# Optimization experiments

Hardware: AMD Instinct MI355X
Metric: run time of the kernel (lower is better)

Reference implementation:

```python
import jax, jax.numpy as jnp
import numpy as np

B, E, N, NREL, K, T, L = 8, 2000, 10000, 25, 16, 3, 32
TAU1 = 10.0

def _clip01(x):
    return jnp.clip(x, 0.0, 1.0)

def setup_inputs():
    key = jax.random.key(0)
    ks = jax.random.split(key, 10)
    ent = jax.random.randint(ks[0], (B,), 0, E)
    input_x = jnp.zeros((B, E), jnp.float32).at[jnp.arange(B), ent].set(1.0)
    tidx = jax.random.randint(ks[1], (E,), 0, K)
    type_mat = jnp.zeros((E, K), jnp.float32).at[jnp.arange(E), tidx].set(1.0)
    heads = jax.random.randint(ks[2], (N,), 0, E)
    tails = jax.random.randint(ks[3], (N,), 0, E)
    rels = jax.random.randint(ks[4], (N,), 0, NREL)
    e2triple = jnp.zeros((E, N), jnp.float32).at[heads, jnp.arange(N)].set(1.0)
    triple2e = jnp.zeros((N, E), jnp.float32).at[jnp.arange(N), tails].set(1.0)
    triple2r = jnp.zeros((N, NREL), jnp.float32).at[jnp.arange(N), rels].set(1.0)
    def ku(k, shape):
        fan_in = int(np.prod(shape[1:]))
        bnd = 1.0 / np.sqrt(fan_in)
        return jax.random.uniform(k, shape, jnp.float32, -bnd, bnd)
    w = ku(ks[5], (T, L, NREL))
    weight = ku(ks[6], (L, 1))
    h = jnp.ones((T, L, NREL - 1), jnp.float32)
    h_x = jnp.ones((L, NREL - 1), jnp.float32)
    h_type = ku(ks[7], (T, L, K))
    h_x_type = ku(ks[8], (L, K))
    alpha = jnp.ones((T, L), jnp.float32)
    beta = jnp.ones((T, L), jnp.float32)
    alpha_x = jnp.ones((L,), jnp.float32)
    beta_x = jnp.ones((L,), jnp.float32)
    return dict(input_x=input_x, type_mat=type_mat, e2triple=e2triple,
                triple2e=triple2e, triple2r=triple2r, w=w, weight=weight,
                h=h, h_x=h_x, h_type=h_type, h_x_type=h_x_type,
                alpha=alpha, beta=beta, alpha_x=alpha_x, beta_x=beta_x, flag=0)

def _forward(input_x, type_mat, e2triple, triple2e, triple2r, w, weight,
             h, h_x, h_type, h_x_type, alpha, beta, alpha_x, beta_x):
    # flag=False, is_training=False path of TCLMModel.forward
    Bb = input_x.shape[0]
    Nn, Ee = triple2e.shape
    Tt, Ll = alpha.shape
    nrel = w.shape[-1]
    half = (nrel - 1) // 2
    x_ori = input_x @ e2triple                      # [B,N]
    e2r = triple2e.T @ triple2r                     # [E,nrel]
    hidden_base = _clip01(e2r)[:, :-1]              # [E,nrel-1]
    hx_raw = _clip01(x_ori @ triple2r)              # [B,nrel]
    hidden_x_base = jnp.concatenate([hx_raw[:, half:-1], hx_raw[:, :half]], axis=-1)
    ax = _clip01(alpha_x / TAU1)
    bx = _clip01(beta_x / TAU1)
    gate_x = 1.0 - _clip01(ax + bx)                 # [L]
    hxp = _clip01(h_x / TAU1)                       # [L,nrel-1]
    hxtp = _clip01(h_x_type / TAU1)                 # [L,K]
    hidden_type_x = input_x @ (type_mat @ hxtp.T)   # [B,L]
    hx_lin = hidden_x_base @ hxp.T                  # [B,L]
    s = None
    for t in range(Tt):
        a = _clip01(alpha[t] / TAU1)                # [L]
        b = _clip01(beta[t] / TAU1)
        hp = _clip01(h[t] / TAU1)                   # [L,nrel-1]
        htp = _clip01(h_type[t] / TAU1)             # [L,K]
        hidden = _clip01(a[None] * (type_mat @ htp.T) + b[None] * (hidden_base @ hp.T))
        hidden = (hidden + (1.0 - _clip01(a + b))[None]).T        # [L,E]
        # note: original code uses alpha/beta (not alpha_x/beta_x) here; replicate
        hidden_x = _clip01(a[None] * hidden_type_x + b[None] * hx_lin) + gate_x[None]  # [B,L]
        w_probs = jax.nn.softmax(w[t], axis=-1)     # [L,nrel]
        srel = triple2r @ w_probs.T                 # [N,L]
        if t == 0:
            sc = x_ori[:, None, :] * srel.T[None]   # [B,L,N]
            s = (sc.reshape(-1, Nn) @ triple2e).reshape(Bb, Ll, Ee)
            s = s * hidden[None] * hidden_x[:, :, None]
        else:
            xprev = (s.reshape(-1, Ee) @ e2triple).reshape(Bb, Ll, Nn)
            sc = xprev * srel.T[None]               # [B,L,N]
            s = (sc.reshape(-1, Nn) @ triple2e).reshape(Bb, Ll, Ee)
            s = s * hidden[None]
    out = jnp.einsum('ble,lk->bek', s, jnp.tanh(weight))[..., 0]  # [B,E]
    return out

def reference(input_x, type_mat, e2triple, triple2e, triple2r, w, weight,
              h, h_x, h_type, h_x_type, alpha, beta, alpha_x, beta_x, flag):
    return _forward(input_x, type_mat, e2triple, triple2e, triple2r, w, weight,
                    h, h_x, h_type, h_x_type, alpha, beta, alpha_x, beta_x)
```

## Files before the change

### kernel.cpp

```cpp
#include <hip/hip_runtime.h>

#define B 8
#define E 2000
#define NTRI 10000
#define NRELS 25
#define KT 16
#define TT 3
#define LL 32
#define TAU1 10.0f

__device__ __forceinline__ float clip01(float x) { return fminf(fmaxf(x, 0.0f), 1.0f); }

__global__ void extract_all(const float4* __restrict__ e2t, const float4* __restrict__ t2e,
                            const float* __restrict__ t2r, const float4* __restrict__ ix,
                            const float4* __restrict__ tm,
                            unsigned int* __restrict__ packed, unsigned int* __restrict__ mask,
                            int* __restrict__ ent, int* __restrict__ tidx,
                            float4* __restrict__ out4) {
    const int gtid = blockIdx.x * blockDim.x + threadIdx.x;
    const int gs = gridDim.x * blockDim.x;

    for (int i = gtid; i < E * NTRI / 4; i += gs) {
        float4 v = e2t[i];
        if (v.x != 0.0f || v.y != 0.0f || v.z != 0.0f || v.w != 0.0f) {
            int f = i * 4;
#pragma unroll
            for (int k = 0; k < 4; k++) {
                float c = (k == 0) ? v.x : (k == 1) ? v.y : (k == 2) ? v.z : v.w;
                if (c != 0.0f) {
                    int a = f + k;
                    int head = a / NTRI;
                    int j = a - head * NTRI;
                    atomicOr(&packed[j], (unsigned int)head);
                }
            }
        }
    }

    for (int i = gtid; i < NTRI * E / 4; i += gs) {
        float4 v = t2e[i];
        if (v.x != 0.0f || v.y != 0.0f || v.z != 0.0f || v.w != 0.0f) {
            int f = i * 4;
#pragma unroll
            for (int k = 0; k < 4; k++) {
                float c = (k == 0) ? v.x : (k == 1) ? v.y : (k == 2) ? v.z : v.w;
                if (c != 0.0f) {
                    int a = f + k;
                    int j = a / E;
                    int tail = a - j * E;
                    int r = 0;
                    while (r < NRELS - 1 && t2r[j * NRELS + r] == 0.0f) r++;
                    atomicOr(&packed[j], ((unsigned int)tail << 11) | ((unsigned int)r << 22));
                    if (r < NRELS - 1) atomicOr(&mask[tail], 1u << r);
                }
            }
        }
    }

    for (int i = gtid; i < B * E / 4; i += gs) {
        float4 v = ix[i];
        if (v.x != 0.0f || v.y != 0.0f || v.z != 0.0f || v.w != 0.0f) {
            int f = i * 4;
#pragma unroll
            for (int k = 0; k < 4; k++) {
                float c = (k == 0) ? v.x : (k == 1) ? v.y : (k == 2) ? v.z : v.w;
                if (c != 0.0f) { int a = f + k; int b = a / E; ent[b] = a - b * E; }
            }
        }
    }

    for (int i = gtid; i < E * KT / 4; i += gs) {
        float4 v = tm[i];
        if (v.x != 0.0f || v.y != 0.0f || v.z != 0.0f || v.w != 0.0f) {
            int f = i * 4;
#pragma unroll
            for (int k = 0; k < 4; k++) {
                float c = (k == 0) ? v.x : (k == 1) ? v.y : (k == 2) ? v.z : v.w;
                if (c != 0.0f) { int a = f + k; int e = a / KT; tidx[e] = a - e * KT; }
            }
        }
    }

    float4 z = make_float4(0.f, 0.f, 0.f, 0.f);
    for (int i = gtid; i < B * E / 4; i += gs) out4[i] = z;
}

__global__ void __launch_bounds__(256) prop(
        const float* __restrict__ sprev, const unsigned int* __restrict__ packed,
        const int* __restrict__ ent, const int* __restrict__ tidx,
        const unsigned int* __restrict__ mask,
        const float* __restrict__ w, const float* __restrict__ h,
        const float* __restrict__ h_type, const float* __restrict__ alpha,
        const float* __restrict__ beta, const float* __restrict__ h_x,
        const float* __restrict__ h_x_type, const float* __restrict__ alpha_x,
        const float* __restrict__ beta_x, const float* __restrict__ weight,
        float* __restrict__ sout, float* __restrict__ out, int t) {
    __shared__ float prev[E];
    __shared__ float acc[E];
    __shared__ float wrow[NRELS];
    __shared__ float hp[NRELS - 1];
    __shared__ float htpL[KT];
    __shared__ unsigned int relflag;

    const int blk = blockIdx.x, b = blk >> 5, l = blk & 31, tid = threadIdx.x;
    const int ent_b = ent[b];
    const int tl = t * LL + l;

    if (t != 0) {
        const float* sp = sprev + (size_t)blk * E;
        for (int e = tid; e < E; e += 256) prev[e] = sp[e];
    }
    for (int e = tid; e < E; e += 256) acc[e] = 0.0f;
    if (tid == 0) {
        relflag = 0u;
        const float* wr = w + tl * NRELS;
        float mx = wr[0];
        for (int r = 1; r < NRELS; r++) mx = fmaxf(mx, wr[r]);
        float ex[NRELS], s = 0.0f;
        for (int r = 0; r < NRELS; r++) { ex[r] = expf(wr[r] - mx); s += ex[r]; }
        float inv = 1.0f / s;
        for (int r = 0; r < NRELS; r++) wrow[r] = ex[r] * inv;
    }
    if (tid < NRELS - 1) hp[tid] = clip01(h[tl * (NRELS - 1) + tid] / TAU1);
    if (tid < KT) htpL[tid] = clip01(h_type[tl * KT + tid] / TAU1);
    __syncthreads();

    const uint4* p4 = (const uint4*)packed;
    if (t == 0) {
        for (int i = tid; i < NTRI / 4; i += 256) {
            uint4 p = p4[i];
#pragma unroll
            for (int k = 0; k < 4; k++) {
                unsigned int pk = (k == 0) ? p.x : (k == 1) ? p.y : (k == 2) ? p.z : p.w;
                int head = pk & 2047;
                if (head == ent_b) {
                    unsigned int r = pk >> 22;
                    int tail = (pk >> 11) & 2047;
                    atomicAdd(&acc[tail], wrow[r]);
                    atomicOr(&relflag, 1u << r);
                }
            }
        }
    } else {
        for (int i = tid; i < NTRI / 4; i += 256) {
            uint4 p = p4[i];
#pragma unroll
            for (int k = 0; k < 4; k++) {
                unsigned int pk = (k == 0) ? p.x : (k == 1) ? p.y : (k == 2) ? p.z : p.w;
                float pv = prev[pk & 2047];
                if (pv != 0.0f) {
                    unsigned int r = pk >> 22;
                    int tail = (pk >> 11) & 2047;
                    atomicAdd(&acc[tail], pv * wrow[r]);
                }
            }
        }
    }
    __syncthreads();

    const float a = clip01(alpha[tl] / TAU1);
    const float bb = clip01(beta[tl] / TAU1);
    const float base = 1.0f - clip01(a + bb);

    float extra = 1.0f;
    if (t == 0) {
        unsigned int fl = relflag;
        float hxlin = 0.0f;
        for (int i = 0; i < NRELS - 1; i++) {
            int pi = (i < 12) ? (12 + i) : (i - 12);
            if ((fl >> pi) & 1u) hxlin += clip01(h_x[l * (NRELS - 1) + i] / TAU1);
        }
        float htx = clip01(h_x_type[l * KT + tidx[ent_b]] / TAU1);
        float ax = clip01(alpha_x[l] / TAU1), bx = clip01(beta_x[l] / TAU1);
        extra = clip01(a * htx + bb * hxlin) + (1.0f - clip01(ax + bx));
    }

    if (t == 2) {
        float tw = tanhf(weight[l]);
        for (int e = tid; e < E; e += 256) {
            unsigned int m = mask[e];
            float dot = 0.0f;
#pragma unroll
            for (int i = 0; i < NRELS - 1; i++) dot += ((m >> i) & 1u) ? hp[i] : 0.0f;
            float he = clip01(a * htpL[tidx[e]] + bb * dot) + base;
            atomicAdd(&out[b * E + e], acc[e] * he * tw);
        }
    } else {
        float* so = sout + (size_t)blk * E;
        for (int e = tid; e < E; e += 256) {
            unsigned int m = mask[e];
            float dot = 0.0f;
#pragma unroll
            for (int i = 0; i < NRELS - 1; i++) dot += ((m >> i) & 1u) ? hp[i] : 0.0f;
            float he = clip01(a * htpL[tidx[e]] + bb * dot) + base;
            so[e] = acc[e] * he * extra;
        }
    }
}

extern "C" void kernel_launch(void* const* d_in, const int* in_sizes, int n_in,
                              void* d_out, int out_size, void* d_ws, size_t ws_size,
                              hipStream_t stream) {
    const float* input_x  = (const float*)d_in[0];
    const float* type_mat = (const float*)d_in[1];
    const float* e2triple = (const float*)d_in[2];
    const float* triple2e = (const float*)d_in[3];
    const float* triple2r = (const float*)d_in[4];
    const float* w        = (const float*)d_in[5];
    const float* weight   = (const float*)d_in[6];
    const float* h        = (const float*)d_in[7];
    const float* h_x      = (const float*)d_in[8];
    const float* h_type   = (const float*)d_in[9];
    const float* h_x_type = (const float*)d_in[10];
    const float* alpha    = (const float*)d_in[11];
    const float* beta     = (const float*)d_in[12];
    const float* alpha_x  = (const float*)d_in[13];
    const float* beta_x   = (const float*)d_in[14];
    (void)in_sizes; (void)n_in; (void)out_size; (void)ws_size;

    char* ws = (char*)d_ws;
    size_t off = 0;
    auto alloc = [&](size_t bytes) -> void* {
        void* p = ws + off;
        off += (bytes + 255) & ~(size_t)255;
        return p;
    };
    unsigned int* packed = (unsigned int*)alloc(NTRI * sizeof(unsigned int));
    unsigned int* maskp  = (unsigned int*)alloc(E * sizeof(unsigned int));
    size_t zero_bytes = off;
    int*   ent  = (int*)alloc(B * sizeof(int));
    int*   tidx = (int*)alloc(E * sizeof(int));
    float* sA   = (float*)alloc((size_t)B * LL * E * sizeof(float));
    float* sB   = (float*)alloc((size_t)B * LL * E * sizeof(float));

    hipMemsetAsync(ws, 0, zero_bytes, stream);

    extract_all<<<8192, 256, 0, stream>>>((const float4*)e2triple, (const float4*)triple2e,
                                          triple2r, (const float4*)input_x, (const float4*)type_mat,
                                          packed, maskp, ent, tidx, (float4*)d_out);

    prop<<<B * LL, 256, 0, stream>>>(nullptr, packed, ent, tidx, maskp, w, h, h_type,
                                     alpha, beta, h_x, h_x_type, alpha_x, beta_x, weight,
                                     sA, (float*)d_out, 0);
    prop<<<B * LL, 256, 0, stream>>>(sA, packed, ent, tidx, maskp, w, h, h_type,
                                     alpha, beta, h_x, h_x_type, alpha_x, beta_x, weight,
                                     sB, (float*)d_out, 1);
    prop<<<B * LL, 256, 0, stream>>>(sB, packed, ent, tidx, maskp, w, h, h_type,
                                     alpha, beta, h_x, h_x_type, alpha_x, beta_x, weight,
                                     nullptr, (float*)d_out, 2);
}
```

Baseline: 250.1 us.

## Fuse three propagation hops into one kernel and batch extraction loads

Merges the three per-hop propagation launches into a single kernel in which each (batch, rule) block keeps its state vector in shared memory across hops. This removes the global round trips through the intermediate state buffers and two kernel launches. Entity masks and type indices are now cached in shared memory, and blocks grow to 512 threads. The extraction kernel now uses fewer blocks, with each thread issuing four independent float4 loads per iteration to raise memory-level parallelism over the large dense matrices. The extra shared memory per block may limit occupancy.

```diff
diff --git a/kernel.cpp b/kernel.cpp
--- a/kernel.cpp
+++ b/kernel.cpp
@@ -8,193 +8,227 @@
 #define TT 3
 #define LL 32
 #define TAU1 10.0f
+#define XBLK 2048
+#define XTHR 256
 
 __device__ __forceinline__ float clip01(float x) { return fminf(fmaxf(x, 0.0f), 1.0f); }
 
-__global__ void extract_all(const float4* __restrict__ e2t, const float4* __restrict__ t2e,
-                            const float* __restrict__ t2r, const float4* __restrict__ ix,
-                            const float4* __restrict__ tm,
-                            unsigned int* __restrict__ packed, unsigned int* __restrict__ mask,
-                            int* __restrict__ ent, int* __restrict__ tidx,
-                            float4* __restrict__ out4) {
-    const int gtid = blockIdx.x * blockDim.x + threadIdx.x;
-    const int gs = gridDim.x * blockDim.x;
-
-    for (int i = gtid; i < E * NTRI / 4; i += gs) {
-        float4 v = e2t[i];
-        if (v.x != 0.0f || v.y != 0.0f || v.z != 0.0f || v.w != 0.0f) {
-            int f = i * 4;
-#pragma unroll
-            for (int k = 0; k < 4; k++) {
-                float c = (k == 0) ? v.x : (k == 1) ? v.y : (k == 2) ? v.z : v.w;
-                if (c != 0.0f) {
-                    int a = f + k;
-                    int head = a / NTRI;
-                    int j = a - head * NTRI;
-                    atomicOr(&packed[j], (unsigned int)head);
-                }
-            }
-        }
-    }
-
-    for (int i = gtid; i < NTRI * E / 4; i += gs) {
-        float4 v = t2e[i];
-        if (v.x != 0.0f || v.y != 0.0f || v.z != 0.0f || v.w != 0.0f) {
-            int f = i * 4;
-#pragma unroll
-            for (int k = 0; k < 4; k++) {
-                float c = (k == 0) ? v.x : (k == 1) ? v.y : (k == 2) ? v.z : v.w;
-                if (c != 0.0f) {
-                    int a = f + k;
-                    int j = a / E;
-                    int tail = a - j * E;
-                    int r = 0;
-                    while (r < NRELS - 1 && t2r[j * NRELS + r] == 0.0f) r++;
-                    atomicOr(&packed[j], ((unsigned int)tail << 11) | ((unsigned int)r << 22));
-                    if (r < NRELS - 1) atomicOr(&mask[tail], 1u << r);
-                }
-            }
-        }
-    }
+__device__ __forceinline__ void proc_e2t(float4 v, int i, unsigned int* packed) {
+    if (v.x == 0.f && v.y == 0.f && v.z == 0.f && v.w == 0.f) return;
+    int f = i * 4;
+    float c[4] = {v.x, v.y, v.z, v.w};
+#pragma unroll
+    for (int k = 0; k < 4; k++)
+        if (c[k] != 0.f) {
+            int a = f + k;
+            int head = a / NTRI;
+            int j = a - head * NTRI;
+            atomicOr(&packed[j], (unsigned int)head);
+        }
+}
+
+__device__ __forceinline__ void proc_t2e(float4 v, int i, const float* __restrict__ t2r,
+                                         unsigned int* packed, unsigned int* mask) {
+    if (v.x == 0.f && v.y == 0.f && v.z == 0.f && v.w == 0.f) return;
+    int f = i * 4;
+    float c[4] = {v.x, v.y, v.z, v.w};
+#pragma unroll
+    for (int k = 0; k < 4; k++)
+        if (c[k] != 0.f) {
+            int a = f + k;
+            int j = a / E;
+            int tail = a - j * E;
+            const float* row = t2r + j * NRELS;
+            int r = 0;
+            while (r < NRELS - 1 && row[r] == 0.f) r++;
+            atomicOr(&packed[j], ((unsigned int)tail << 11) | ((unsigned int)r << 22));
+            if (r < NRELS - 1) atomicOr(&mask[tail], 1u << r);
+        }
+}
+
+__global__ void __launch_bounds__(XTHR) extract_all(
+        const float4* __restrict__ e2t, const float4* __restrict__ t2e,
+        const float* __restrict__ t2r, const float4* __restrict__ ix,
+        const float4* __restrict__ tm,
+        unsigned int* __restrict__ packed, unsigned int* __restrict__ mask,
+        int* __restrict__ ent, int* __restrict__ tidx, float4* __restrict__ out4) {
+    const int gtid = blockIdx.x * XTHR + threadIdx.x;
+    const int gs = XBLK * XTHR;
 
     for (int i = gtid; i < B * E / 4; i += gs) {
         float4 v = ix[i];
-        if (v.x != 0.0f || v.y != 0.0f || v.z != 0.0f || v.w != 0.0f) {
+        if (v.x != 0.f || v.y != 0.f || v.z != 0.f || v.w != 0.f) {
             int f = i * 4;
-#pragma unroll
-            for (int k = 0; k < 4; k++) {
-                float c = (k == 0) ? v.x : (k == 1) ? v.y : (k == 2) ? v.z : v.w;
-                if (c != 0.0f) { int a = f + k; int b = a / E; ent[b] = a - b * E; }
-            }
-        }
-    }
-
+            float c[4] = {v.x, v.y, v.z, v.w};
+#pragma unroll
+            for (int k = 0; k < 4; k++)
+                if (c[k] != 0.f) { int a = f + k; int b = a / E; ent[b] = a - b * E; }
+        }
+    }
     for (int i = gtid; i < E * KT / 4; i += gs) {
         float4 v = tm[i];
-        if (v.x != 0.0f || v.y != 0.0f || v.z != 0.0f || v.w != 0.0f) {
+        if (v.x != 0.f || v.y != 0.f || v.z != 0.f || v.w != 0.f) {
             int f = i * 4;
-#pragma unroll
-            for (int k = 0; k < 4; k++) {
-                float c = (k == 0) ? v.x : (k == 1) ? v.y : (k == 2) ? v.z : v.w;
-                if (c != 0.0f) { int a = f + k; int e = a / KT; tidx[e] = a - e * KT; }
-            }
-        }
-    }
-
+            float c[4] = {v.x, v.y, v.z, v.w};
+#pragma unroll
+            for (int k = 0; k < 4; k++)
+                if (c[k] != 0.f) { int a = f + k; int e = a / KT; tidx[e] = a - e * KT; }
+        }
+    }
     float4 z = make_float4(0.f, 0.f, 0.f, 0.f);
     for (int i = gtid; i < B * E / 4; i += gs) out4[i] = z;
-}
-
-__global__ void __launch_bounds__(256) prop(
-        const float* __restrict__ sprev, const unsigned int* __restrict__ packed,
-        const int* __restrict__ ent, const int* __restrict__ tidx,
-        const unsigned int* __restrict__ mask,
+
+    {
+        const int n4 = E * NTRI / 4;
+        for (int i0 = gtid; i0 < n4; i0 += gs * 4) {
+            int i1 = i0 + gs, i2 = i0 + 2 * gs, i3 = i0 + 3 * gs;
+            float4 v0 = e2t[i0];
+            float4 v1 = (i1 < n4) ? e2t[i1] : z;
+            float4 v2 = (i2 < n4) ? e2t[i2] : z;
+            float4 v3 = (i3 < n4) ? e2t[i3] : z;
+            proc_e2t(v0, i0, packed);
+            proc_e2t(v1, i1, packed);
+            proc_e2t(v2, i2, packed);
+            proc_e2t(v3, i3, packed);
+        }
+    }
+    {
+        const int n4 = NTRI * E / 4;
+        for (int i0 = gtid; i0 < n4; i0 += gs * 4) {
+            int i1 = i0 + gs, i2 = i0 + 2 * gs, i3 = i0 + 3 * gs;
+            float4 v0 = t2e[i0];
+            float4 v1 = (i1 < n4) ? t2e[i1] : z;
+            float4 v2 = (i2 < n4) ? t2e[i2] : z;
+            float4 v3 = (i3 < n4) ? t2e[i3] : z;
+            proc_t2e(v0, i0, t2r, packed, mask);
+            proc_t2e(v1, i1, t2r, packed, mask);
+            proc_t2e(v2, i2, t2r, packed, mask);
+            proc_t2e(v3, i3, t2r, packed, mask);
+        }
+    }
+}
+
+__global__ void __launch_bounds__(512) mega_prop(
+        const unsigned int* __restrict__ packed, const int* __restrict__ ent,
+        const int* __restrict__ tidx, const unsigned int* __restrict__ mask,
         const float* __restrict__ w, const float* __restrict__ h,
         const float* __restrict__ h_type, const float* __restrict__ alpha,
         const float* __restrict__ beta, const float* __restrict__ h_x,
         const float* __restrict__ h_x_type, const float* __restrict__ alpha_x,
         const float* __restrict__ beta_x, const float* __restrict__ weight,
-        float* __restrict__ sout, float* __restrict__ out, int t) {
+        float* __restrict__ out) {
     __shared__ float prev[E];
     __shared__ float acc[E];
+    __shared__ unsigned int mask_s[E];
+    __shared__ int tidx_s[E];
     __shared__ float wrow[NRELS];
     __shared__ float hp[NRELS - 1];
     __shared__ float htpL[KT];
     __shared__ unsigned int relflag;
-
+    __shared__ float extra_s;
+
+    const int NT = 512;
     const int blk = blockIdx.x, b = blk >> 5, l = blk & 31, tid = threadIdx.x;
     const int ent_b = ent[b];
-    const int tl = t * LL + l;
-
-    if (t != 0) {
-        const float* sp = sprev + (size_t)blk * E;
-        for (int e = tid; e < E; e += 256) prev[e] = sp[e];
-    }
-    for (int e = tid; e < E; e += 256) acc[e] = 0.0f;
-    if (tid == 0) {
-        relflag = 0u;
-        const float* wr = w + tl * NRELS;
-        float mx = wr[0];
-        for (int r = 1; r < NRELS; r++) mx = fmaxf(mx, wr[r]);
-        float ex[NRELS], s = 0.0f;
-        for (int r = 0; r < NRELS; r++) { ex[r] = expf(wr[r] - mx); s += ex[r]; }
-        float inv = 1.0f / s;
-        for (int r = 0; r < NRELS; r++) wrow[r] = ex[r] * inv;
-    }
-    if (tid < NRELS - 1) hp[tid] = clip01(h[tl * (NRELS - 1) + tid] / TAU1);
-    if (tid < KT) htpL[tid] = clip01(h_type[tl * KT + tid] / TAU1);
-    __syncthreads();
+
+    for (int e = tid; e < E; e += NT) {
+        acc[e] = 0.f;
+        mask_s[e] = mask[e];
+        tidx_s[e] = tidx[e];
+    }
+    if (tid == 0) { relflag = 0u; extra_s = 1.f; }
 
     const uint4* p4 = (const uint4*)packed;
-    if (t == 0) {
-        for (int i = tid; i < NTRI / 4; i += 256) {
-            uint4 p = p4[i];
-#pragma unroll
-            for (int k = 0; k < 4; k++) {
-                unsigned int pk = (k == 0) ? p.x : (k == 1) ? p.y : (k == 2) ? p.z : p.w;
-                int head = pk & 2047;
-                if (head == ent_b) {
-                    unsigned int r = pk >> 22;
-                    int tail = (pk >> 11) & 2047;
-                    atomicAdd(&acc[tail], wrow[r]);
-                    atomicOr(&relflag, 1u << r);
+
+    for (int t = 0; t < TT; t++) {
+        const int tl = t * LL + l;
+        if (tid == 0) {
+            const float* wr = w + tl * NRELS;
+            float mx = wr[0];
+            for (int r = 1; r < NRELS; r++) mx = fmaxf(mx, wr[r]);
+            float ex[NRELS], s = 0.f;
+            for (int r = 0; r < NRELS; r++) { ex[r] = expf(wr[r] - mx); s += ex[r]; }
+            float inv = 1.f / s;
+            for (int r = 0; r < NRELS; r++) wrow[r] = ex[r] * inv;
+        }
+        if (tid >= 64 && tid < 64 + NRELS - 1)
+            hp[tid - 64] = clip01(h[tl * (NRELS - 1) + (tid - 64)] / TAU1);
+        if (tid >= 128 && tid < 128 + KT)
+            htpL[tid - 128] = clip01(h_type[tl * KT + (tid - 128)] / TAU1);
+        __syncthreads();
+
+        if (t == 0) {
+            for (int i = tid; i < NTRI / 4; i += NT) {
+                uint4 p = p4[i];
+#pragma unroll
+                for (int k = 0; k < 4; k++) {
+                    unsigned int pk = (k == 0) ? p.x : (k == 1) ? p.y : (k == 2) ? p.z : p.w;
+                    if ((int)(pk & 2047u) == ent_b) {
+                        unsigned int r = pk >> 22;
+                        int tail = (pk >> 11) & 2047;
+                        atomicAdd(&acc[tail], wrow[r]);
+                        atomicOr(&relflag, 1u << r);
+                    }
                 }
             }
-        }
-    } else {
-        for (int i = tid; i < NTRI / 4; i += 256) {
-            uint4 p = p4[i];
-#pragma unroll
-            for (int k = 0; k < 4; k++) {
-                unsigned int pk = (k == 0) ? p.x : (k == 1) ? p.y : (k == 2) ? p.z : p.w;
-                float pv = prev[pk & 2047];
-                if (pv != 0.0f) {
-                    unsigned int r = pk >> 22;
-                    int tail = (pk >> 11) & 2047;
-                    atomicAdd(&acc[tail], pv * wrow[r]);
+        } else {
+            for (int i = tid; i < NTRI / 4; i += NT) {
+                uint4 p = p4[i];
+#pragma unroll
+                for (int k = 0; k < 4; k++) {
+                    unsigned int pk = (k == 0) ? p.x : (k == 1) ? p.y : (k == 2) ? p.z : p.w;
+                    float pv = prev[pk & 2047u];
+                    if (pv != 0.f) {
+                        unsigned int r = pk >> 22;
+                        int tail = (pk >> 11) & 2047;
+                        atomicAdd(&acc[tail], pv * wrow[r]);
+                    }
                 }
             }
         }
-    }
-    __syncthreads();
-
-    const float a = clip01(alpha[tl] / TAU1);
-    const float bb = clip01(beta[tl] / TAU1);
-    const float base = 1.0f - clip01(a + bb);
-
-    float extra = 1.0f;
-    if (t == 0) {
-        unsigned int fl = relflag;
-        float hxlin = 0.0f;
-        for (int i = 0; i < NRELS - 1; i++) {
-            int pi = (i < 12) ? (12 + i) : (i - 12);
-            if ((fl >> pi) & 1u) hxlin += clip01(h_x[l * (NRELS - 1) + i] / TAU1);
-        }
-        float htx = clip01(h_x_type[l * KT + tidx[ent_b]] / TAU1);
-        float ax = clip01(alpha_x[l] / TAU1), bx = clip01(beta_x[l] / TAU1);
-        extra = clip01(a * htx + bb * hxlin) + (1.0f - clip01(ax + bx));
-    }
-
-    if (t == 2) {
-        float tw = tanhf(weight[l]);
-        for (int e = tid; e < E; e += 256) {
-            unsigned int m = mask[e];
-            float dot = 0.0f;
-#pragma unroll
-            for (int i = 0; i < NRELS - 1; i++) dot += ((m >> i) & 1u) ? hp[i] : 0.0f;
-            float he = clip01(a * htpL[tidx[e]] + bb * dot) + base;
-            atomicAdd(&out[b * E + e], acc[e] * he * tw);
-        }
-    } else {
-        float* so = sout + (size_t)blk * E;
-        for (int e = tid; e < E; e += 256) {
-            unsigned int m = mask[e];
-            float dot = 0.0f;
-#pragma unroll
-            for (int i = 0; i < NRELS - 1; i++) dot += ((m >> i) & 1u) ? hp[i] : 0.0f;
-            float he = clip01(a * htpL[tidx[e]] + bb * dot) + base;
-            so[e] = acc[e] * he * extra;
-        }
+        __syncthreads();
+
+        const float a = clip01(alpha[tl] / TAU1);
+        const float bb = clip01(beta[tl] / TAU1);
+        const float base = 1.f - clip01(a + bb);
+
+        if (t == 0 && tid == 0) {
+            unsigned int fl = relflag;
+            float hxlin = 0.f;
+            for (int i = 0; i < NRELS - 1; i++) {
+                int pi = (i < 12) ? (12 + i) : (i - 12);
+                if ((fl >> pi) & 1u) hxlin += clip01(h_x[l * (NRELS - 1) + i] / TAU1);
+            }
+            float htx = clip01(h_x_type[l * KT + tidx_s[ent_b]] / TAU1);
+            float ax = clip01(alpha_x[l] / TAU1), bx = clip01(beta_x[l] / TAU1);
+            extra_s = clip01(a * htx + bb * hxlin) + (1.f - clip01(ax + bx));
+        }
+        __syncthreads();
+
+        const float extra = (t == 0) ? extra_s : 1.f;
+
+        if (t < TT - 1) {
+            for (int e = tid; e < E; e += NT) {
+                unsigned int m = mask_s[e];
+                float dot = 0.f;
+#pragma unroll
+                for (int i = 0; i < NRELS - 1; i++) dot += ((m >> i) & 1u) ? hp[i] : 0.f;
+                float he = clip01(a * htpL[tidx_s[e]] + bb * dot) + base;
+                prev[e] = acc[e] * he * extra;
+                acc[e] = 0.f;
+            }
+        } else {
+            float tw = tanhf(weight[l]);
+            for (int e = tid; e < E; e += NT) {
+                unsigned int m = mask_s[e];
+                float dot = 0.f;
+#pragma unroll
+                for (int i = 0; i < NRELS - 1; i++) dot += ((m >> i) & 1u) ? hp[i] : 0.f;
+                float he = clip01(a * htpL[tidx_s[e]] + bb * dot) + base;
+                atomicAdd(&out[b * E + e], acc[e] * he * tw);
+            }
+        }
+        __syncthreads();
     }
 }
 
@@ -228,24 +262,17 @@
     unsigned int* packed = (unsigned int*)alloc(NTRI * sizeof(unsigned int));
     unsigned int* maskp  = (unsigned int*)alloc(E * sizeof(unsigned int));
     size_t zero_bytes = off;
-    int*   ent  = (int*)alloc(B * sizeof(int));
-    int*   tidx = (int*)alloc(E * sizeof(int));
-    float* sA   = (float*)alloc((size_t)B * LL * E * sizeof(float));
-    float* sB   = (float*)alloc((size_t)B * LL * E * sizeof(float));
+    int* ent  = (int*)alloc(B * sizeof(int));
+    int* tidx = (int*)alloc(E * sizeof(int));
 
     hipMemsetAsync(ws, 0, zero_bytes, stream);
 
-    extract_all<<<8192, 256, 0, stream>>>((const float4*)e2triple, (const float4*)triple2e,
-                                          triple2r, (const float4*)input_x, (const float4*)type_mat,
-                                          packed, maskp, ent, tidx, (float4*)d_out);
-
-    prop<<<B * LL, 256, 0, stream>>>(nullptr, packed, ent, tidx, maskp, w, h, h_type,
-                                     alpha, beta, h_x, h_x_type, alpha_x, beta_x, weight,
-                                     sA, (float*)d_out, 0);
-    prop<<<B * LL, 256, 0, stream>>>(sA, packed, ent, tidx, maskp, w, h, h_type,
-                                     alpha, beta, h_x, h_x_type, alpha_x, beta_x, weight,
-                                     sB, (float*)d_out, 1);
-    prop<<<B * LL, 256, 0, stream>>>(sB, packed, ent, tidx, maskp, w, h, h_type,
-                                     alpha, beta, h_x, h_x_type, alpha_x, beta_x, weight,
-                                     nullptr, (float*)d_out, 2);
-}
+    extract_all<<<XBLK, XTHR, 0, stream>>>((const float4*)e2triple, (const float4*)triple2e,
+                                           triple2r, (const float4*)input_x,
+                                           (const float4*)type_mat,
+                                           packed, maskp, ent, tidx, (float4*)d_out);
+
+    mega_prop<<<B * LL, 512, 0, stream>>>(packed, ent, tidx, maskp, w, h, h_type,
+                                          alpha, beta, h_x, h_x_type, alpha_x, beta_x,
+                                          weight, (float*)d_out);
+}
```

Measured after the change: 244.0 us. 2.4% less time.
